# Performance work log

Hardware: AMD Instinct MI355X
Metric: run time of the kernel (lower is better)

## Reference

```python
import jax, jax.numpy as jnp
import numpy as np

D_MODEL = 256
NCODES = 32


def setup_inputs() -> dict:
    key = jax.random.key(0)
    k1, k2 = jax.random.split(key)
    B, L = 64, 2048
    rev_repr = jax.random.normal(k1, (B, L, D_MODEL), dtype=jnp.float32)
    # xavier_normal for Linear(256 -> ncodes): std = sqrt(2/(fan_in+fan_out))
    std = (2.0 / (D_MODEL + NCODES)) ** 0.5
    W_codes = jax.random.normal(k2, (NCODES, D_MODEL), dtype=jnp.float32) * std
    return {"rev_repr": rev_repr, "W_codes": W_codes}


def reference(rev_repr, W_codes):
    # scores: (B, L, ncodes) = rev_repr @ W_codes.T
    scores = jnp.einsum('bld,kd->blk', rev_repr, W_codes)
    # softmax over the L (sequence) dimension, dim=1
    wts = jax.nn.softmax(scores, axis=1)
    # fused weighted-sum pooling: (B, ncodes, 256) — avoids (B,L,ncodes,256) intermediate
    contexts = jnp.einsum('blk,bld->bkd', wts, rev_repr)
    return contexts
```

## Files before the change

### kernel.cpp

```cpp
#include <hip/hip_runtime.h>
#include <math.h>

#define BATCH 64
#define LSEQ 2048
#define DMOD 256
#define KC 32
#define LCHUNK 256
#define LS 32
#define NSUB 8
#define PITCH_D 264
#define PITCH_L 40

typedef __bf16 bf16x8 __attribute__((ext_vector_type(8)));
typedef __bf16 bf16x4 __attribute__((ext_vector_type(4)));
typedef float f32x4 __attribute__((ext_vector_type(4)));

__global__ __launch_bounds__(256, 2) void fused_pool_kernel(
    const float* __restrict__ rev, const float* __restrict__ W,
    float* __restrict__ cPartial, float* __restrict__ zPartial) {
  __shared__ __align__(16) __bf16 sW[KC * PITCH_D];
  __shared__ __align__(16) __bf16 sRev[LS * PITCH_D];
  __shared__ __align__(16) __bf16 sRevT[DMOD * PITCH_L];
  __shared__ __align__(16) __bf16 sP[KC * PITCH_L];
  __shared__ float sZw[2][KC];

  const int tid = threadIdx.x;
  const int b = blockIdx.y;
  const int lc = blockIdx.x;
  const int lbase = lc * LCHUNK;
  const int wave = tid >> 6;
  const int lane = tid & 63;
  const int col = lane & 15;
  const int quad = lane >> 4;

  const int Mt = wave & 1;
  const int Nt = wave >> 1;

#pragma unroll
  for (int i = 0; i < 8; ++i) {
    int flat = tid + 256 * i;
    int kk = flat >> 6, c4 = flat & 63;
    float4 v = *(const float4*)(W + kk * DMOD + c4 * 4);
    bf16x4 h = {(__bf16)v.x, (__bf16)v.y, (__bf16)v.z, (__bf16)v.w};
    *(bf16x4*)(&sW[kk * PITCH_D + c4 * 4]) = h;
  }

  f32x4 acc2[8];
#pragma unroll
  for (int i = 0; i < 8; ++i) acc2[i] = (f32x4){0.f, 0.f, 0.f, 0.f};
  float zacc[4] = {0.f, 0.f, 0.f, 0.f};

  for (int sub = 0; sub < NSUB; ++sub) {
    const int l0 = lbase + sub * LS;
    __syncthreads();
#pragma unroll
    for (int i = 0; i < 8; ++i) {
      int slot = tid + 256 * i;
      int r = slot >> 6, c4 = slot & 63;
      float4 v = *(const float4*)(rev + ((size_t)b * LSEQ + l0 + r) * DMOD + c4 * 4);
      bf16x4 h = {(__bf16)v.x, (__bf16)v.y, (__bf16)v.z, (__bf16)v.w};
      *(bf16x4*)(&sRev[r * PITCH_D + c4 * 4]) = h;
    }
    __syncthreads();

#pragma unroll
    for (int j4 = 0; j4 < 4; ++j4) {
      bf16x8 v;
#pragma unroll
      for (int j = 0; j < 8; ++j) v[j] = sRev[(j4 * 8 + j) * PITCH_D + tid];
      *(bf16x8*)(&sRevT[tid * PITCH_L + j4 * 8]) = v;
    }

    f32x4 acc1 = {0.f, 0.f, 0.f, 0.f};
#pragma unroll
    for (int ks = 0; ks < 8; ++ks) {
      bf16x8 afrag = *(const bf16x8*)(&sW[(Mt * 16 + col) * PITCH_D + ks * 32 + quad * 8]);
      bf16x8 bfrag = *(const bf16x8*)(&sRev[(Nt * 16 + col) * PITCH_D + ks * 32 + quad * 8]);
      acc1 = __builtin_amdgcn_mfma_f32_16x16x32_bf16(afrag, bfrag, acc1, 0, 0, 0);
    }
#pragma unroll
    for (int reg = 0; reg < 4; ++reg) {
      float p = __expf(acc1[reg]);
      __bf16 ph = (__bf16)p;
      zacc[reg] += (float)ph;
      sP[(Mt * 16 + quad * 4 + reg) * PITCH_L + Nt * 16 + col] = ph;
    }
    __syncthreads();

    bf16x8 pa = *(const bf16x8*)(&sP[(Mt * 16 + col) * PITCH_L + quad * 8]);
#pragma unroll
    for (int nt = 0; nt < 8; ++nt) {
      int dt = Nt * 8 + nt;
      bf16x8 bb = *(const bf16x8*)(&sRevT[(dt * 16 + col) * PITCH_L + quad * 8]);
      acc2[nt] = __builtin_amdgcn_mfma_f32_16x16x32_bf16(pa, bb, acc2[nt], 0, 0, 0);
    }
  }

#pragma unroll
  for (int off = 1; off < 16; off <<= 1)
#pragma unroll
    for (int reg = 0; reg < 4; ++reg) zacc[reg] += __shfl_xor(zacc[reg], off, 64);
  if (col == 0) {
#pragma unroll
    for (int reg = 0; reg < 4; ++reg)
      sZw[Nt][Mt * 16 + quad * 4 + reg] = zacc[reg];
  }
  __syncthreads();
  if (tid < KC)
    zPartial[((size_t)b * 8 + lc) * KC + tid] = sZw[0][tid] + sZw[1][tid];

  float* dst = cPartial + (((size_t)b * 8 + lc) * KC) * DMOD;
#pragma unroll
  for (int nt = 0; nt < 8; ++nt) {
    int d = (Nt * 8 + nt) * 16 + col;
#pragma unroll
    for (int reg = 0; reg < 4; ++reg) {
      int k = Mt * 16 + quad * 4 + reg;
      dst[k * DMOD + d] = acc2[nt][reg];
    }
  }
}

__global__ __launch_bounds__(256) void reduce_kernel(
    const float* __restrict__ cPartial, const float* __restrict__ zPartial,
    float* __restrict__ out) {
  int idx = blockIdx.x * 256 + threadIdx.x;
  int b = idx >> 13;
  int k = (idx >> 8) & 31;
  int d = idx & 255;
  float s = 0.f, z = 0.f;
#pragma unroll
  for (int lcc = 0; lcc < 8; ++lcc) {
    s += cPartial[(((size_t)b * 8 + lcc) * KC + k) * DMOD + d];
    z += zPartial[((size_t)b * 8 + lcc) * KC + k];
  }
  out[idx] = s / z;
}

extern "C" void kernel_launch(void* const* d_in, const int* in_sizes, int n_in,
                              void* d_out, int out_size, void* d_ws,
                              size_t ws_size, hipStream_t stream) {
  const float* rev = (const float*)d_in[0];
  const float* W = (const float*)d_in[1];
  float* out = (float*)d_out;

  float* ws = (float*)d_ws;
  float* cPartial = ws;
  float* zPartial = cPartial + (size_t)BATCH * 8 * KC * DMOD;

  fused_pool_kernel<<<dim3(8, BATCH), dim3(256), 0, stream>>>(rev, W, cPartial,
                                                              zPartial);
  reduce_kernel<<<dim3(2048), dim3(256), 0, stream>>>(cPartial, zPartial, out);
}
```

Measured before the change: 196.8 us.

## Prefetch next rev sub-tile into registers and vectorize reduce kernel

The fused kernel now issues the global loads for the next 32-row sub-tile into registers right after the current tile is staged to shared memory, so the load latency overlaps with the transpose and MFMA work of the current tile. The reduce kernel is changed to process four contiguous outputs per thread with float4 loads and stores and a reciprocal multiply, launching a quarter as many blocks. The prefetch adds 32 live float registers per thread, which raises register pressure and may conflict with the two-blocks-per-SM launch bound.

```diff
diff --git a/kernel.cpp b/kernel.cpp
--- a/kernel.cpp
+++ b/kernel.cpp
@@ -28,8 +28,8 @@
   const int b = blockIdx.y;
   const int lc = blockIdx.x;
   const int lbase = lc * LCHUNK;
+  const int lane = tid & 63;
   const int wave = tid >> 6;
-  const int lane = tid & 63;
   const int col = lane & 15;
   const int quad = lane >> 4;
 
@@ -50,18 +50,36 @@
   for (int i = 0; i < 8; ++i) acc2[i] = (f32x4){0.f, 0.f, 0.f, 0.f};
   float zacc[4] = {0.f, 0.f, 0.f, 0.f};
 
+  float4 pf[8];
+#pragma unroll
+  for (int i = 0; i < 8; ++i) {
+    int slot = tid + 256 * i;
+    int r = slot >> 6, c4 = slot & 63;
+    pf[i] = *(const float4*)(rev + ((size_t)b * LSEQ + lbase + r) * DMOD + c4 * 4);
+  }
+
   for (int sub = 0; sub < NSUB; ++sub) {
-    const int l0 = lbase + sub * LS;
     __syncthreads();
+
 #pragma unroll
     for (int i = 0; i < 8; ++i) {
       int slot = tid + 256 * i;
       int r = slot >> 6, c4 = slot & 63;
-      float4 v = *(const float4*)(rev + ((size_t)b * LSEQ + l0 + r) * DMOD + c4 * 4);
+      float4 v = pf[i];
       bf16x4 h = {(__bf16)v.x, (__bf16)v.y, (__bf16)v.z, (__bf16)v.w};
       *(bf16x4*)(&sRev[r * PITCH_D + c4 * 4]) = h;
     }
     __syncthreads();
+
+    if (sub + 1 < NSUB) {
+      const int l1 = lbase + (sub + 1) * LS;
+#pragma unroll
+      for (int i = 0; i < 8; ++i) {
+        int slot = tid + 256 * i;
+        int r = slot >> 6, c4 = slot & 63;
+        pf[i] = *(const float4*)(rev + ((size_t)b * LSEQ + l1 + r) * DMOD + c4 * 4);
+      }
+    }
 
 #pragma unroll
     for (int j4 = 0; j4 < 4; ++j4) {
@@ -125,16 +143,20 @@
     const float* __restrict__ cPartial, const float* __restrict__ zPartial,
     float* __restrict__ out) {
   int idx = blockIdx.x * 256 + threadIdx.x;
-  int b = idx >> 13;
-  int k = (idx >> 8) & 31;
-  int d = idx & 255;
-  float s = 0.f, z = 0.f;
+  int b = idx >> 11;
+  int k = (idx >> 6) & 31;
+  float4 s = {0.f, 0.f, 0.f, 0.f};
+  float z = 0.f;
 #pragma unroll
   for (int lcc = 0; lcc < 8; ++lcc) {
-    s += cPartial[(((size_t)b * 8 + lcc) * KC + k) * DMOD + d];
+    const float4 v = *(const float4*)(cPartial + ((((size_t)b * 8 + lcc) * KC + k) << 8) +
+                                      ((idx & 63) << 2));
+    s.x += v.x; s.y += v.y; s.z += v.z; s.w += v.w;
     z += zPartial[((size_t)b * 8 + lcc) * KC + k];
   }
-  out[idx] = s / z;
+  float zi = 1.0f / z;
+  float4 o = {s.x * zi, s.y * zi, s.z * zi, s.w * zi};
+  *(float4*)(out + ((size_t)idx << 2)) = o;
 }
 
 extern "C" void kernel_launch(void* const* d_in, const int* in_sizes, int n_in,
@@ -150,5 +172,5 @@
 
   fused_pool_kernel<<<dim3(8, BATCH), dim3(256), 0, stream>>>(rev, W, cPartial,
                                                               zPartial);
-  reduce_kernel<<<dim3(2048), dim3(256), 0, stream>>>(cPartial, zPartial, out);
+  reduce_kernel<<<dim3(512), dim3(256), 0, stream>>>(cPartial, zPartial, out);
 }
```

Result: no change. 197.3 us (+0.3%).
